# Kernel tuning notes

Measured on AMD Instinct MI355X. Metric: run time of the kernel, lower is better.

The kernel has to match this reference:

```python
import jax, jax.numpy as jnp
import numpy as np

T, N, XD, H, Z, E = 6, 4096, 64, 256, 128, 131072


def setup_inputs() -> dict:
    key = jax.random.key(0)
    ks = jax.random.split(key, 16)
    f32 = jnp.float32
    def rn(k, shp):
        return jax.random.normal(k, shp, f32)
    def gl(k, shp):  # glorot-ish init, scaled by fan_in
        return jax.random.normal(k, shp, f32) * np.float32(1.0 / np.sqrt(shp[-2]))
    return {
        "x": rn(ks[0], (T, N, XD)),
        "edges": jax.random.randint(ks[1], (T, 2, E), 0, N, dtype=jnp.int32),
        "eps": rn(ks[2], (T, N, Z)),
        "drop_u": jax.random.uniform(ks[3], (T, N, Z), f32),
        "phi_x_w": gl(ks[4], (XD, H)), "phi_x_b": jnp.zeros((H,), f32),
        "phi_z_w": gl(ks[5], (Z, H)), "phi_z_b": jnp.zeros((H,), f32),
        "enc_w": gl(ks[6], (2 * H, H)),
        "enc_mu_w": gl(ks[7], (H, Z)),
        "enc_lv_w": gl(ks[8], (H, Z)),
        "prior_w": gl(ks[9], (H, H)), "prior_b": jnp.zeros((H,), f32),
        "prior_mu_w": gl(ks[10], (H, Z)), "prior_mu_b": jnp.zeros((Z,), f32),
        "prior_lv_w": gl(ks[11], (H, Z)), "prior_lv_b": jnp.zeros((Z,), f32),
        "gru_wx": gl(ks[12], (4, 2 * H, H)),  # gates i,f,o,c; x-side GCN weights
        "gru_wh": gl(ks[13], (4, H, H)),      # gates i,f,o,c; h-side GCN weights
    }


def reference(x, edges, eps, drop_u, phi_x_w, phi_x_b, phi_z_w, phi_z_b,
              enc_w, enc_mu_w, enc_lv_w, prior_w, prior_b,
              prior_mu_w, prior_mu_b, prior_lv_w, prior_lv_b,
              gru_wx, gru_wh):
    T_, N_, _ = x.shape
    H_ = phi_x_w.shape[1]
    h = jnp.zeros((N_, H_), x.dtype)
    c = jnp.zeros((N_, H_), x.dtype)
    loop = jnp.arange(N_, dtype=edges.dtype)
    enc_mus, prior_mus = [], []
    dec_t = None
    for t in range(T_):  # fixed small T; edge structure differs per step
        row = jnp.concatenate([edges[t, 0], loop])  # add self loops
        col = jnp.concatenate([edges[t, 1], loop])
        deg = jax.ops.segment_sum(jnp.ones(row.shape, x.dtype), row, num_segments=N_)
        dinv = jnp.where(deg > 0, jax.lax.rsqrt(deg), jnp.zeros((), x.dtype))
        norm = (dinv[row] * dinv[col])[:, None]

        def gcn(xx, W):
            # GCNConv: xW, gather at col, scale by sym-norm, scatter-add at row
            return jax.ops.segment_sum(norm * (xx @ W)[col], row, num_segments=N_)

        phi_x_t = jax.nn.relu(x[t] @ phi_x_w + phi_x_b)
        enc_t = jax.nn.relu(gcn(jnp.concatenate([phi_x_t, h], axis=1), enc_w))
        enc_mu_t = gcn(enc_t, enc_mu_w)
        enc_std_t = jax.nn.softplus(gcn(enc_t, enc_lv_w))
        prior_t = jax.nn.relu(h @ prior_w + prior_b)
        prior_mu_t = prior_t @ prior_mu_w + prior_mu_b
        _prior_std_t = jax.nn.softplus(prior_t @ prior_lv_w + prior_lv_b)  # computed as in original, unused in returns
        z_t = eps[t] * enc_std_t + enc_mu_t  # original: eps.mul(logvar).add_(mu)
        phi_z_t = jax.nn.relu(z_t @ phi_z_w + phi_z_b)
        # InnerProductDecoder with dropout(p=0.5, training=True), identity act
        z_drop = jnp.where(drop_u[t] < 0.5, z_t * 2.0, jnp.zeros((), x.dtype))
        dec_t = z_drop @ z_drop.T  # [N, N]
        # graph-LSTM step (n_layer = 1)
        xin = jnp.concatenate([phi_x_t, phi_z_t], axis=1)  # [N, 2H]
        gi = jax.nn.sigmoid(gcn(xin, gru_wx[0]) + gcn(h, gru_wh[0]))
        gf = jax.nn.sigmoid(gcn(xin, gru_wx[1]) + gcn(h, gru_wh[1]))
        go = jax.nn.sigmoid(gcn(xin, gru_wx[2]) + gcn(h, gru_wh[2]))
        ct = jnp.tanh(gcn(xin, gru_wx[3]) + gcn(h, gru_wh[3]))
        c_new = gf * h + gi * ct    # faithful to original: F_g * h[i] (not c)
        h_new = go * jnp.tanh(c)    # faithful to original: uses old c[i]
        h, c = h_new, c_new
        enc_mus.append(enc_mu_t)
        prior_mus.append(prior_mu_t)
    return jnp.stack(enc_mus), jnp.stack(prior_mus), h[None], dec_t
```

## Files before the change

kernel.cpp:

```cpp
#include <hip/hip_runtime.h>
#include <hip/hip_bf16.h>
#include <math.h>

#define T_  6
#define NN  4096
#define XD_ 64
#define H_  256
#define ZZ  128
#define EE  131072

typedef unsigned short u16;
typedef __attribute__((ext_vector_type(8))) short short8;
typedef __attribute__((ext_vector_type(8))) unsigned short u16x8;
typedef __attribute__((ext_vector_type(4))) float f32x4;

__device__ __forceinline__ float bf2f(u16 u) { return __uint_as_float(((unsigned)u) << 16); }
__device__ __forceinline__ u16 f2bf(float f) {
    unsigned x = __float_as_uint(f);
    return (u16)((x + 0x7FFFu + ((x >> 16) & 1u)) >> 16);
}

__global__ void k_deg(const int* __restrict__ edges, int* __restrict__ degcnt) {
    int t = blockIdx.y;
    int e = blockIdx.x * 256 + threadIdx.x;
    const int* rows = edges + (size_t)t * 2 * EE;
    atomicAdd(&degcnt[t * NN + rows[e]], 1);
}

__global__ void k_scan_dinv(const int* __restrict__ degcnt_all,
                            int* __restrict__ row_start_all,
                            int* __restrict__ cursor_all,
                            float* __restrict__ dinv_all) {
    __shared__ int sbuf[1024];
    int tt = blockIdx.x;
    const int* degcnt = degcnt_all + tt * NN;
    int* row_start = row_start_all + tt * (NN + 1);
    int* cursor = cursor_all + tt * NN;
    float* dinv = dinv_all + tt * NN;
    int t = threadIdx.x;
    int b = t * 4;
    int v0 = degcnt[b + 0], v1 = degcnt[b + 1], v2 = degcnt[b + 2], v3 = degcnt[b + 3];
    dinv[b + 0] = rsqrtf((float)(v0 + 1));
    dinv[b + 1] = rsqrtf((float)(v1 + 1));
    dinv[b + 2] = rsqrtf((float)(v2 + 1));
    dinv[b + 3] = rsqrtf((float)(v3 + 1));
    int s = v0 + v1 + v2 + v3;
    sbuf[t] = s;
    __syncthreads();
    for (int off = 1; off < 1024; off <<= 1) {
        int x = sbuf[t];
        int y = (t >= off) ? sbuf[t - off] : 0;
        __syncthreads();
        sbuf[t] = x + y;
        __syncthreads();
    }
    int excl = sbuf[t] - s;
    int r0 = excl, r1 = excl + v0, r2 = r1 + v1, r3 = r2 + v2;
    row_start[b + 0] = r0; cursor[b + 0] = r0;
    row_start[b + 1] = r1; cursor[b + 1] = r1;
    row_start[b + 2] = r2; cursor[b + 2] = r2;
    row_start[b + 3] = r3; cursor[b + 3] = r3;
    if (t == 1023) row_start[NN] = r3 + v3;
}

__global__ void k_scatter(const int* __restrict__ edges,
                          int* __restrict__ cursor, const float* __restrict__ dinv,
                          int* __restrict__ col_idx, float* __restrict__ val) {
    int t = blockIdx.y;
    int e = blockIdx.x * 256 + threadIdx.x;
    const int* rows = edges + (size_t)t * 2 * EE;
    const int* cols = rows + EE;
    int r = rows[e], cc = cols[e];
    int pos = atomicAdd(&cursor[t * NN + r], 1);
    col_idx[(size_t)t * EE + pos] = cc;
    val[(size_t)t * EE + pos] = dinv[t * NN + r] * dinv[t * NN + cc];
}

__device__ __forceinline__ void sp_row_wave(const u16* __restrict__ Y,
                                            const int* __restrict__ row_start,
                                            const int* __restrict__ col_idx,
                                            const float* __restrict__ val,
                                            const float* __restrict__ dinv,
                                            u16* __restrict__ outp, int ldo, int r) {
    int lane = threadIdx.x & 63;
    int half = lane >> 5;
    int cg = lane & 31;
    int s0 = row_start[r], s1 = row_start[r + 1];
    float a[8] = {0.f, 0.f, 0.f, 0.f, 0.f, 0.f, 0.f, 0.f};
    for (int base = s0; base < s1; base += 64) {
        int n = s1 - base; if (n > 64) n = 64;
        int cl = 0; float vl = 0.f;
        if (base + lane < s1) { cl = col_idx[base + lane]; vl = val[base + lane]; }
        for (int e = 0; e < n; e += 2) {
            int ei = e + half;
            int cc = __shfl(cl, ei);
            float v = (ei < n) ? __shfl(vl, ei) : 0.f;
            u16x8 y = *(const u16x8*)(Y + (size_t)cc * H_ + cg * 8);
#pragma unroll
            for (int j = 0; j < 8; ++j) a[j] += v * bf2f(y[j]);
        }
    }
#pragma unroll
    for (int j = 0; j < 8; ++j) a[j] += __shfl_xor(a[j], 32);
    if (half == 0) {
        float dr = dinv[r], sc = dr * dr;
        u16x8 ys = *(const u16x8*)(Y + (size_t)r * H_ + cg * 8);
        u16x8 o;
#pragma unroll
        for (int j = 0; j < 8; ++j) o[j] = f2bf(a[j] + sc * bf2f(ys[j]));
        *(u16x8*)(outp + (size_t)r * ldo + cg * 8) = o;
    }
}

__global__ void k_spmm(const u16* __restrict__ Y1,
                       const int* __restrict__ row_start_all, const int* __restrict__ col_idx_all,
                       const float* __restrict__ val_all, const float* __restrict__ dinv_all,
                       u16* __restrict__ out1, int ldo,
                       long long sY, long long sO) {
    int t = blockIdx.y;
    int w = threadIdx.x >> 6;
    sp_row_wave(Y1 + (size_t)t * sY, row_start_all + (size_t)t * (NN + 1),
                col_idx_all + (size_t)t * EE, val_all + (size_t)t * EE,
                dinv_all + (size_t)t * NN, out1 + (size_t)t * sO, ldo,
                blockIdx.x * 4 + w);
}

template<int MF>
__device__ __forceinline__ void mm_core(const u16* __restrict__ A, int lda,
                                        const u16* __restrict__ BT, int ldbt, int K,
                                        int row0, int col0,
                                        f32x4 acc[MF][MF], char* smem) {
    constexpr int TILE = MF * 32;
    u16* As = (u16*)smem;
    u16* Bs = As + TILE * 64;
    const int lane = threadIdx.x & 63;
    const int w = threadIdx.x >> 6;
    const int wr = (w >> 1) * (TILE / 2);
    const int wc = (w & 1) * (TILE / 2);

    int gRow[MF], gCol[MF];
#pragma unroll
    for (int i = 0; i < MF; ++i) {
        int G = (w * MF + i) * 64 + lane;
        int r = G >> 3;
        gRow[i] = r;
        gCol[i] = ((G & 7) ^ (r & 7)) << 3;
    }

    for (int k0 = 0; k0 < K; k0 += 64) {
#pragma unroll
        for (int i = 0; i < MF; ++i) {
            const u16* sa = A + (size_t)(row0 + gRow[i]) * lda + k0 + gCol[i];
            __builtin_amdgcn_global_load_lds(
                (const __attribute__((address_space(1))) void*)sa,
                (__attribute__((address_space(3))) void*)(As + (w * MF + i) * 512), 16, 0, 0);
            const u16* sb = BT + (size_t)(col0 + gRow[i]) * ldbt + k0 + gCol[i];
            __builtin_amdgcn_global_load_lds(
                (const __attribute__((address_space(1))) void*)sb,
                (__attribute__((address_space(3))) void*)(Bs + (w * MF + i) * 512), 16, 0, 0);
        }
        __syncthreads();
#pragma unroll
        for (int kk = 0; kk < 2; ++kk) {
            short8 a[MF], b[MF];
#pragma unroll
            for (int mf = 0; mf < MF; ++mf) {
                int r = wr + mf * 16 + (lane & 15);
                int off = (r * 128 + kk * 64 + (lane >> 4) * 16) ^ ((r & 7) << 4);
                a[mf] = *(const short8*)((const char*)As + off);
            }
#pragma unroll
            for (int nf = 0; nf < MF; ++nf) {
                int r = wc + nf * 16 + (lane & 15);
                int off = (r * 128 + kk * 64 + (lane >> 4) * 16) ^ ((r & 7) << 4);
                b[nf] = *(const short8*)((const char*)Bs + off);
            }
#pragma unroll
            for (int mf = 0; mf < MF; ++mf)
#pragma unroll
                for (int nf = 0; nf < MF; ++nf)
                    acc[mf][nf] = __builtin_amdgcn_mfma_f32_16x16x32_bf16(
                        a[mf], b[nf], acc[mf][nf], 0, 0, 0);
        }
        __syncthreads();
    }
}

template<int MF>
__launch_bounds__(256)
__global__ void k_mm(const u16* __restrict__ A, int lda,
                     const u16* __restrict__ BT, int ldbt, int K,
                     float* __restrict__ C0, int ldc0,
                     u16* __restrict__ C1, int ldc1,
                     const float* __restrict__ bias, int act,
                     float* __restrict__ C2,
                     const float* __restrict__ du, u16* __restrict__ zdOut) {
    constexpr int TILE = MF * 32;
    constexpr int STAGE_B = TILE * 64 * 2 * 2;
    constexpr int EPI_B = (MF == 2) ? 64 * 68 * 4 : 0;
    constexpr int SMEM_B = STAGE_B > EPI_B ? STAGE_B : EPI_B;
    __shared__ alignas(16) char smem[SMEM_B];

    const int tid = threadIdx.x;
    const int lane = tid & 63;
    const int w = tid >> 6;
    const int row0 = blockIdx.y * TILE;
    const int col0 = blockIdx.x * TILE;
    const int wr = (w >> 1) * (TILE / 2);
    const int wc = (w & 1) * (TILE / 2);

    f32x4 acc[MF][MF];
#pragma unroll
    for (int i = 0; i < MF; ++i)
#pragma unroll
        for (int j = 0; j < MF; ++j)
            acc[i][j] = f32x4{0.f, 0.f, 0.f, 0.f};

    mm_core<MF>(A, lda, BT, ldbt, K, row0, col0, acc, smem);

    const int ci = lane & 15;
    const int ri = (lane >> 4) * 4;

    if constexpr (MF == 2) {
        if (act == 4) {
            float (*epi)[68] = (float(*)[68])smem;
#pragma unroll
            for (int mf = 0; mf < 2; ++mf)
#pragma unroll
                for (int nf = 0; nf < 2; ++nf)
#pragma unroll
                    for (int i = 0; i < 4; ++i)
                        epi[wr + mf * 16 + ri + i][wc + nf * 16 + ci] = acc[mf][nf][i];
            __syncthreads();
            float* muo = C0; const float* eps = C2; u16* zo = C1;
#pragma unroll
            for (int k = 0; k < 8; ++k) {
                int p = tid + k * 256;
                int row = p >> 5, jl = p & 31;
                float mu = epi[row][jl * 2];
                float sp = epi[row][jl * 2 + 1];
                float sd = (sp > 20.f) ? sp : log1pf(expf(sp));
                int idx = (row0 + row) * ZZ + (col0 >> 1) + jl;
                muo[idx] = mu;
                u16 z16 = f2bf(eps[idx] * sd + mu);
                zo[idx] = z16;
                if (zdOut)
                    zdOut[idx] = (du[idx] < 0.5f) ? f2bf(2.f * bf2f(z16)) : (u16)0;
            }
            return;
        }
    }

#pragma unroll
    for (int mf = 0; mf < MF; ++mf) {
#pragma unroll
        for (int nf = 0; nf < MF; ++nf) {
            int row = row0 + wr + mf * 16 + ri;
            int col = col0 + wc + nf * 16 + ci;
            if (C1) {
                float bv = bias ? bias[col] : 0.f;
#pragma unroll
                for (int i = 0; i < 4; ++i) {
                    float v = acc[mf][nf][i] + bv;
                    if (act == 1) v = fmaxf(v, 0.f);
                    C1[(size_t)(row + i) * ldc1 + col] = f2bf(v);
                }
            } else {
                float bv = bias ? bias[col] : 0.f;
#pragma unroll
                for (int i = 0; i < 4; ++i)
                    C0[(size_t)(row + i) * ldc0 + col] = acc[mf][nf][i] + bv;
            }
        }
    }
}

__launch_bounds__(256)
__global__ void k_dual(const u16* __restrict__ A0, int lda0, const u16* __restrict__ BT0,
                       int ldbt0, int K0, u16* __restrict__ Cb0, int ldcb0,
                       const u16* __restrict__ A1, int lda1, const u16* __restrict__ BT1,
                       int ldbt1, int K1, float* __restrict__ Cf1, int ldcf1,
                       const float* __restrict__ bias1) {
    __shared__ alignas(16) char smem[16384];
    const int z = blockIdx.z;
    if (z && blockIdx.x >= 2) return;
    const u16* A = z ? A1 : A0;   int lda = z ? lda1 : lda0;
    const u16* BT = z ? BT1 : BT0; int ldbt = z ? ldbt1 : ldbt0;
    int K = z ? K1 : K0;

    const int lane = threadIdx.x & 63;
    const int w = threadIdx.x >> 6;
    const int row0 = blockIdx.y * 64;
    const int col0 = blockIdx.x * 64;
    const int wr = (w >> 1) * 32, wc = (w & 1) * 32;

    f32x4 acc[2][2];
#pragma unroll
    for (int i = 0; i < 2; ++i)
#pragma unroll
        for (int j = 0; j < 2; ++j) acc[i][j] = f32x4{0.f, 0.f, 0.f, 0.f};
    mm_core<2>(A, lda, BT, ldbt, K, row0, col0, acc, smem);

    const int ci = lane & 15, ri = (lane >> 4) * 4;
#pragma unroll
    for (int mf = 0; mf < 2; ++mf)
#pragma unroll
        for (int nf = 0; nf < 2; ++nf) {
            int row = row0 + wr + mf * 16 + ri;
            int col = col0 + wc + nf * 16 + ci;
            if (z == 0) {
#pragma unroll
                for (int i = 0; i < 4; ++i)
                    Cb0[(size_t)(row + i) * ldcb0 + col] = f2bf(fmaxf(acc[mf][nf][i], 0.f));
            } else {
                float bv = bias1[col];
#pragma unroll
                for (int i = 0; i < 4; ++i)
                    Cf1[(size_t)(row + i) * ldcf1 + col] = acc[mf][nf][i] + bv;
            }
        }
}

__launch_bounds__(256)
__global__ void k_sp_mm(const u16* __restrict__ Y, const int* __restrict__ row_start,
                        const int* __restrict__ col_idx, const float* __restrict__ val,
                        const float* __restrict__ dinv, u16* __restrict__ spOut, int spLdo,
                        int doSp,
                        const u16* __restrict__ A, int lda, const u16* __restrict__ BT,
                        int ldbt, int K, float* __restrict__ Cf, int ldcf,
                        u16* __restrict__ Cb, int ldcb,
                        const float* __restrict__ bias, int gx) {
    __shared__ alignas(16) char smem[16384];
    int bid = blockIdx.x;
    if (bid < NN / 4) {
        if (!doSp) return;
        int w = threadIdx.x >> 6;
        sp_row_wave(Y, row_start, col_idx, val, dinv, spOut, spLdo, bid * 4 + w);
        return;
    }
    int b2 = bid - NN / 4;
    const int row0 = (b2 / gx) * 64;
    const int col0 = (b2 % gx) * 64;
    const int lane = threadIdx.x & 63;
    const int w = threadIdx.x >> 6;
    const int wr = (w >> 1) * 32, wc = (w & 1) * 32;
    f32x4 acc[2][2];
#pragma unroll
    for (int i = 0; i < 2; ++i)
#pragma unroll
        for (int j = 0; j < 2; ++j) acc[i][j] = f32x4{0.f, 0.f, 0.f, 0.f};
    mm_core<2>(A, lda, BT, ldbt, K, row0, col0, acc, smem);
    const int ci = lane & 15, ri = (lane >> 4) * 4;
#pragma unroll
    for (int mf = 0; mf < 2; ++mf)
#pragma unroll
        for (int nf = 0; nf < 2; ++nf) {
            int row = row0 + wr + mf * 16 + ri;
            int col = col0 + wc + nf * 16 + ci;
            float bv = bias ? bias[col] : 0.f;
            if (Cb) {
#pragma unroll
                for (int i = 0; i < 4; ++i)
                    Cb[(size_t)(row + i) * ldcb + col] = f2bf(fmaxf(acc[mf][nf][i] + bv, 0.f));
            } else {
#pragma unroll
                for (int i = 0; i < 4; ++i)
                    Cf[(size_t)(row + i) * ldcf + col] = acc[mf][nf][i] + bv;
            }
        }
}

__launch_bounds__(256)
__global__ void k_gates(const u16* __restrict__ XIN, const u16* __restrict__ BgT,
                        float* __restrict__ h, float* __restrict__ c,
                        u16* __restrict__ hbf, float* __restrict__ hOut,
                        int skipSH) {
    __shared__ alignas(16) char smem[128 * 68 * 4];
    u16* As = (u16*)smem;
    u16* Bs = As + 128 * 64;
    const int tid = threadIdx.x;
    const int lane = tid & 63;
    const int w = tid >> 6;
    const int row0 = blockIdx.y * 128;
    const int col0 = blockIdx.x * 64;
    const int wrB = (w >> 1) * 64;
    const int wc = (w & 1) * 32;

    f32x4 acc[4][2];
#pragma unroll
    for (int i = 0; i < 4; ++i)
#pragma unroll
        for (int j = 0; j < 2; ++j) acc[i][j] = f32x4{0.f, 0.f, 0.f, 0.f};

    int aRow[4], aCol[4];
#pragma unroll
    for (int i = 0; i < 4; ++i) {
        int G = (w * 4 + i) * 64 + lane;
        int r = G >> 3;
        aRow[i] = r;
        aCol[i] = ((G & 7) ^ (r & 7)) << 3;
    }
    int bRow[2], bCol[2];
#pragma unroll
    for (int i = 0; i < 2; ++i) {
        int G = (w * 2 + i) * 64 + lane;
        int r = G >> 3;
        bRow[i] = r;
        bCol[i] = ((G & 7) ^ (r & 7)) << 3;
    }

    const int nIter = skipSH ? 8 : 12;
    for (int it = 0; it < nIter; ++it) {
        int k0 = it * 64 + ((skipSH && it >= 4) ? 256 : 0);
#pragma unroll
        for (int i = 0; i < 4; ++i) {
            const u16* sa = XIN + (size_t)(row0 + aRow[i]) * 768 + k0 + aCol[i];
            __builtin_amdgcn_global_load_lds(
                (const __attribute__((address_space(1))) void*)sa,
                (__attribute__((address_space(3))) void*)(As + (w * 4 + i) * 512), 16, 0, 0);
        }
#pragma unroll
        for (int i = 0; i < 2; ++i) {
            const u16* sb = BgT + (size_t)(col0 + bRow[i]) * 768 + k0 + bCol[i];
            __builtin_amdgcn_global_load_lds(
                (const __attribute__((address_space(1))) void*)sb,
                (__attribute__((address_space(3))) void*)(Bs + (w * 2 + i) * 512), 16, 0, 0);
        }
        __syncthreads();
#pragma unroll
        for (int kk = 0; kk < 2; ++kk) {
            short8 a[4], b[2];
#pragma unroll
            for (int mf = 0; mf < 4; ++mf) {
                int r = wrB + mf * 16 + (lane & 15);
                int off = (r * 128 + kk * 64 + (lane >> 4) * 16) ^ ((r & 7) << 4);
                a[mf] = *(const short8*)((const char*)As + off);
            }
#pragma unroll
            for (int nf = 0; nf < 2; ++nf) {
                int r = wc + nf * 16 + (lane & 15);
                int off = (r * 128 + kk * 64 + (lane >> 4) * 16) ^ ((r & 7) << 4);
                b[nf] = *(const short8*)((const char*)Bs + off);
            }
#pragma unroll
            for (int mf = 0; mf < 4; ++mf)
#pragma unroll
                for (int nf = 0; nf < 2; ++nf)
                    acc[mf][nf] = __builtin_amdgcn_mfma_f32_16x16x32_bf16(
                        a[mf], b[nf], acc[mf][nf], 0, 0, 0);
        }
        __syncthreads();
    }

    const int ci = lane & 15;
    const int ri = (lane >> 4) * 4;
    float (*epi)[68] = (float(*)[68])smem;
#pragma unroll
    for (int mf = 0; mf < 4; ++mf)
#pragma unroll
        for (int nf = 0; nf < 2; ++nf)
#pragma unroll
            for (int i = 0; i < 4; ++i)
                epi[wrB + mf * 16 + ri + i][wc + nf * 16 + ci] = acc[mf][nf][i];
    __syncthreads();
#pragma unroll
    for (int k = 0; k < 8; ++k) {
        int p = tid + k * 256;
        int row = p >> 4, jl = p & 15;
        float4 g4 = *(const float4*)&epi[row][jl * 4];
        float gi = 1.f / (1.f + expf(-g4.x));
        float gf = 1.f / (1.f + expf(-g4.y));
        float go = 1.f / (1.f + expf(-g4.z));
        float ct = tanhf(g4.w);
        int idx = (row0 + row) * H_ + (col0 >> 2) + jl;
        float ho = h[idx], co = c[idx];
        float cn = gf * ho + gi * ct;
        float hn = go * tanhf(co);
        h[idx] = hn;
        c[idx] = cn;
        hbf[idx] = f2bf(hn);
        if (hOut) hOut[idx] = hn;
    }
}

__global__ void k_cvt(const float* __restrict__ in, u16* __restrict__ outp, int n4) {
    int i = blockIdx.x * 256 + threadIdx.x;
    if (i >= n4) return;
    float4 v = ((const float4*)in)[i];
    ((ushort4*)outp)[i] = make_ushort4(f2bf(v.x), f2bf(v.y), f2bf(v.z), f2bf(v.w));
}

__global__ void k_prep(const float* __restrict__ phi_x_w, const float* __restrict__ phi_z_w,
                       const float* __restrict__ enc_w, const float* __restrict__ prior_w,
                       const float* __restrict__ prior_mu_w,
                       const float* __restrict__ enc_mu_w, const float* __restrict__ enc_lv_w,
                       const float* __restrict__ gru_wx, const float* __restrict__ gru_wh,
                       u16* __restrict__ phi_x_wT, u16* __restrict__ phi_z_wT,
                       u16* __restrict__ enc_wT, u16* __restrict__ prior_wT,
                       u16* __restrict__ prior_mu_wT, u16* __restrict__ mulvT,
                       u16* __restrict__ BgT) {
    int idx = blockIdx.x * 256 + threadIdx.x;
    if (idx < 16384) {
        int j = idx >> 6, k = idx & 63;
        phi_x_wT[idx] = f2bf(phi_x_w[k * 256 + j]);
        return;
    }
    idx -= 16384;
    if (idx < 32768) {
        int j = idx >> 7, k = idx & 127;
        phi_z_wT[idx] = f2bf(phi_z_w[k * 256 + j]);
        return;
    }
    idx -= 32768;
    if (idx < 131072) {
        int j = idx >> 9, k = idx & 511;
        enc_wT[idx] = f2bf(enc_w[k * 256 + j]);
        return;
    }
    idx -= 131072;
    if (idx < 65536) {
        int j = idx >> 8, k = idx & 255;
        prior_wT[idx] = f2bf(prior_w[k * 256 + j]);
        return;
    }
    idx -= 65536;
    if (idx < 32768) {
        int j = idx >> 8, k = idx & 255;
        prior_mu_wT[idx] = f2bf(prior_mu_w[k * 128 + j]);
        return;
    }
    idx -= 32768;
    if (idx < 65536) {
        int cp = idx >> 8, k = idx & 255;
        int j = cp >> 1, s = cp & 1;
        float v = s ? enc_lv_w[k * 128 + j] : enc_mu_w[k * 128 + j];
        mulvT[idx] = f2bf(v);
        return;
    }
    idx -= 65536;
    if (idx < 786432) {
        int cp = idx / 768, k = idx % 768;
        int g = cp & 3, j = cp >> 2;
        float v;
        if (k < 256)      v = gru_wx[((size_t)g * 512 + k) * 256 + j];
        else if (k < 512) v = gru_wh[((size_t)g * 256 + (k - 256)) * 256 + j];
        else              v = gru_wx[((size_t)g * 512 + (k - 256)) * 256 + j];
        BgT[idx] = f2bf(v);
    }
}

extern "C" void kernel_launch(void* const* d_in, const int* in_sizes, int n_in,
                              void* d_out_v, int out_size, void* d_ws, size_t ws_size,
                              hipStream_t stream) {
    (void)in_sizes; (void)n_in; (void)out_size;
    const float* x          = (const float*)d_in[0];
    const int*   edges      = (const int*)d_in[1];
    const float* eps        = (const float*)d_in[2];
    const float* drop_u     = (const float*)d_in[3];
    const float* phi_x_w    = (const float*)d_in[4];
    const float* phi_x_b    = (const float*)d_in[5];
    const float* phi_z_w    = (const float*)d_in[6];
    const float* phi_z_b    = (const float*)d_in[7];
    const float* enc_w      = (const float*)d_in[8];
    const float* enc_mu_w   = (const float*)d_in[9];
    const float* enc_lv_w   = (const float*)d_in[10];
    const float* prior_w    = (const float*)d_in[11];
    const float* prior_b    = (const float*)d_in[12];
    const float* prior_mu_w = (const float*)d_in[13];
    const float* prior_mu_b = (const float*)d_in[14];
    const float* gru_wx     = (const float*)d_in[17];
    const float* gru_wh     = (const float*)d_in[18];
    float* out = (float*)d_out_v;

    char* base = (char*)d_ws;
    size_t cur = 0;
    auto carve = [&](size_t bytes) -> void* {
        void* p = base + cur;
        cur += (bytes + 255) & ~(size_t)255;
        return p;
    };
    float* h         = (float*)carve((size_t)NN * H_ * 4);
    float* c         = (float*)carve((size_t)NN * H_ * 4);
    u16* h_bf        = (u16*)carve((size_t)NN * H_ * 2);
    size_t hcz_bytes = cur;
    float* dinv      = (float*)carve((size_t)T_ * NN * 4);
    int*   degcnt    = (int*)carve((size_t)T_ * NN * 4);
    int*   row_start = (int*)carve((size_t)T_ * (NN + 1) * 4);
    int*   cursor    = (int*)carve((size_t)T_ * NN * 4);
    int*   col_idx   = (int*)carve((size_t)T_ * EE * 4);
    float* val       = (float*)carve((size_t)T_ * EE * 4);
    u16* x_bf        = (u16*)carve((size_t)T_ * NN * XD_ * 2);
    u16* phi6        = (u16*)carve((size_t)T_ * NN * H_ * 2);
    u16* phi         = (u16*)carve((size_t)NN * H_ * 2);
    u16* enc_t       = (u16*)carve((size_t)NN * H_ * 2);
    u16* SEb         = (u16*)carve((size_t)NN * H_ * 2);
    u16* prior_t     = (u16*)carve((size_t)NN * H_ * 2);
    u16* XIN6        = (u16*)carve((size_t)T_ * NN * 768 * 2);
    u16* zbuf        = (u16*)carve((size_t)NN * ZZ * 2);
    u16* zd          = (u16*)carve((size_t)NN * ZZ * 2);
    u16* phi_x_wT    = (u16*)carve((size_t)XD_ * H_ * 2);
    u16* phi_z_wT    = (u16*)carve((size_t)ZZ * H_ * 2);
    u16* enc_wT      = (u16*)carve((size_t)512 * H_ * 2);
    u16* prior_wT    = (u16*)carve((size_t)H_ * H_ * 2);
    u16* prior_mu_wT = (u16*)carve((size_t)ZZ * H_ * 2);
    u16* mulvT       = (u16*)carve((size_t)H_ * H_ * 2);
    u16* BgT         = (u16*)carve((size_t)1024 * 768 * 2);
    if (cur > ws_size) return;

    const size_t NZ = (size_t)NN * ZZ;
    const size_t HOFF = (size_t)2 * T_ * NZ;
    const size_t DECOFF = HOFF + (size_t)NN * H_;

    k_cvt<<<(T_ * NN * XD_ / 4 + 255) / 256, 256, 0, stream>>>(x, x_bf, T_ * NN * XD_ / 4);
    k_prep<<<(1130496 + 255) / 256, 256, 0, stream>>>(
        phi_x_w, phi_z_w, enc_w, prior_w, prior_mu_w, enc_mu_w, enc_lv_w,
        gru_wx, gru_wh,
        phi_x_wT, phi_z_wT, enc_wT, prior_wT, prior_mu_wT, mulvT, BgT);

    hipMemsetAsync(degcnt, 0, (size_t)T_ * NN * 4, stream);
    k_deg<<<dim3(EE / 256, T_), 256, 0, stream>>>(edges, degcnt);
    k_scan_dinv<<<T_, 1024, 0, stream>>>(degcnt, row_start, cursor, dinv);
    k_scatter<<<dim3(EE / 256, T_), 256, 0, stream>>>(edges, cursor, dinv, col_idx, val);

    k_mm<2><<<dim3(4, (T_ * NN) / 64), 256, 0, stream>>>(x_bf, XD_, phi_x_wT, XD_, XD_,
        nullptr, 0, phi6, H_, phi_x_b, 1, nullptr, nullptr, nullptr);
    k_spmm<<<dim3(NN / 4, T_), 256, 0, stream>>>(phi6, row_start, col_idx, val, dinv,
        XIN6, 768, (long long)NN * H_, (long long)NN * 768);

    hipMemsetAsync(h, 0, hcz_bytes, stream);

    for (int t = 0; t < T_; ++t) {
        const int* rs_t = row_start + (size_t)t * (NN + 1);
        const int* ci_t = col_idx + (size_t)t * EE;
        const float* vv_t = val + (size_t)t * EE;
        const float* dv_t = dinv + (size_t)t * NN;
        u16* xin_t = XIN6 + (size_t)t * NN * 768;
        int last = (t == T_ - 1);

        k_sp_mm<<<NN / 4 + 256, 256, 0, stream>>>(h_bf, rs_t, ci_t, vv_t, dv_t,
            xin_t + 256, 768, t > 0,
            h_bf, H_, prior_wT, H_, H_, nullptr, 0, prior_t, H_, prior_b, 4);
        k_dual<<<dim3(4, 64, 2), 256, 0, stream>>>(
            xin_t, 768, enc_wT, 512, (t == 0) ? 256 : 512, enc_t, H_,
            prior_t, H_, prior_mu_wT, H_, H_,
            out + (size_t)(T_ + t) * NZ, ZZ, prior_mu_b);
        k_spmm<<<dim3(NN / 4, 1), 256, 0, stream>>>(enc_t, rs_t, ci_t, vv_t, dv_t,
                                                    SEb, H_, 0, 0);
        k_mm<2><<<dim3(4, 64), 256, 0, stream>>>(SEb, H_, mulvT, H_, H_,
            out + (size_t)t * NZ, 0, zbuf, 0, nullptr, 4, (float*)(eps + (size_t)t * NZ),
            last ? drop_u + (size_t)t * NZ : nullptr, last ? zd : nullptr);
        k_mm<2><<<dim3(4, 64), 256, 0, stream>>>(zbuf, ZZ, phi_z_wT, ZZ, ZZ,
            nullptr, 0, phi, H_, phi_z_b, 1, nullptr, nullptr, nullptr);
        k_spmm<<<dim3(NN / 4, 1), 256, 0, stream>>>(phi, rs_t, ci_t, vv_t, dv_t,
                                                    xin_t + 512, 768, 0, 0);
        k_gates<<<dim3(16, 32), 256, 0, stream>>>(xin_t, BgT, h, c, h_bf,
            last ? out + HOFF : nullptr, t == 0);
    }

    k_mm<4><<<dim3(32, 32), 256, 0, stream>>>(zd, ZZ, zd, ZZ, ZZ,
        out + DECOFF, NN, nullptr, 0, nullptr, 0, nullptr, nullptr, nullptr);
}
```

Baseline: 611.1 us.

## Fuse per-timestep kernel chain into one cooperative persistent kernel with grid syncs

Replaces the sequence of roughly seven kernel launches per timestep with a single cooperative kernel that loops over timesteps and stages, separating stages with grid-wide syncs. It also folds the x conversion and the degree memset into the weight-prep kernel. The aim is to remove launch overhead and inter-kernel gaps across the serial recurrence. The cost is that each stage is limited to a fixed grid of 256 or 512 blocks, grid.sync has its own overhead, and a non-cooperative fallback path is kept.

```diff
diff --git a/kernel.cpp b/kernel.cpp
--- a/kernel.cpp
+++ b/kernel.cpp
@@ -1,6 +1,8 @@
 #include <hip/hip_runtime.h>
-#include <hip/hip_bf16.h>
+#include <hip/hip_cooperative_groups.h>
 #include <math.h>
+
+namespace cg = cooperative_groups;
 
 #define T_  6
 #define NN  4096
@@ -84,7 +86,7 @@
                                             u16* __restrict__ outp, int ldo, int r) {
     int lane = threadIdx.x & 63;
     int half = lane >> 5;
-    int cg = lane & 31;
+    int cg2 = lane & 31;
     int s0 = row_start[r], s1 = row_start[r + 1];
     float a[8] = {0.f, 0.f, 0.f, 0.f, 0.f, 0.f, 0.f, 0.f};
     for (int base = s0; base < s1; base += 64) {
@@ -95,7 +97,7 @@
             int ei = e + half;
             int cc = __shfl(cl, ei);
             float v = (ei < n) ? __shfl(vl, ei) : 0.f;
-            u16x8 y = *(const u16x8*)(Y + (size_t)cc * H_ + cg * 8);
+            u16x8 y = *(const u16x8*)(Y + (size_t)cc * H_ + cg2 * 8);
 #pragma unroll
             for (int j = 0; j < 8; ++j) a[j] += v * bf2f(y[j]);
         }
@@ -104,11 +106,11 @@
     for (int j = 0; j < 8; ++j) a[j] += __shfl_xor(a[j], 32);
     if (half == 0) {
         float dr = dinv[r], sc = dr * dr;
-        u16x8 ys = *(const u16x8*)(Y + (size_t)r * H_ + cg * 8);
+        u16x8 ys = *(const u16x8*)(Y + (size_t)r * H_ + cg2 * 8);
         u16x8 o;
 #pragma unroll
         for (int j = 0; j < 8; ++j) o[j] = f2bf(a[j] + sc * bf2f(ys[j]));
-        *(u16x8*)(outp + (size_t)r * ldo + cg * 8) = o;
+        *(u16x8*)(outp + (size_t)r * ldo + cg2 * 8) = o;
     }
 }
 
@@ -186,170 +188,18 @@
     }
 }
 
-template<int MF>
-__launch_bounds__(256)
-__global__ void k_mm(const u16* __restrict__ A, int lda,
-                     const u16* __restrict__ BT, int ldbt, int K,
-                     float* __restrict__ C0, int ldc0,
-                     u16* __restrict__ C1, int ldc1,
-                     const float* __restrict__ bias, int act,
-                     float* __restrict__ C2,
-                     const float* __restrict__ du, u16* __restrict__ zdOut) {
-    constexpr int TILE = MF * 32;
-    constexpr int STAGE_B = TILE * 64 * 2 * 2;
-    constexpr int EPI_B = (MF == 2) ? 64 * 68 * 4 : 0;
-    constexpr int SMEM_B = STAGE_B > EPI_B ? STAGE_B : EPI_B;
-    __shared__ alignas(16) char smem[SMEM_B];
-
-    const int tid = threadIdx.x;
-    const int lane = tid & 63;
-    const int w = tid >> 6;
-    const int row0 = blockIdx.y * TILE;
-    const int col0 = blockIdx.x * TILE;
-    const int wr = (w >> 1) * (TILE / 2);
-    const int wc = (w & 1) * (TILE / 2);
-
-    f32x4 acc[MF][MF];
-#pragma unroll
-    for (int i = 0; i < MF; ++i)
-#pragma unroll
-        for (int j = 0; j < MF; ++j)
-            acc[i][j] = f32x4{0.f, 0.f, 0.f, 0.f};
-
-    mm_core<MF>(A, lda, BT, ldbt, K, row0, col0, acc, smem);
-
-    const int ci = lane & 15;
-    const int ri = (lane >> 4) * 4;
-
-    if constexpr (MF == 2) {
-        if (act == 4) {
-            float (*epi)[68] = (float(*)[68])smem;
-#pragma unroll
-            for (int mf = 0; mf < 2; ++mf)
-#pragma unroll
-                for (int nf = 0; nf < 2; ++nf)
-#pragma unroll
-                    for (int i = 0; i < 4; ++i)
-                        epi[wr + mf * 16 + ri + i][wc + nf * 16 + ci] = acc[mf][nf][i];
-            __syncthreads();
-            float* muo = C0; const float* eps = C2; u16* zo = C1;
-#pragma unroll
-            for (int k = 0; k < 8; ++k) {
-                int p = tid + k * 256;
-                int row = p >> 5, jl = p & 31;
-                float mu = epi[row][jl * 2];
-                float sp = epi[row][jl * 2 + 1];
-                float sd = (sp > 20.f) ? sp : log1pf(expf(sp));
-                int idx = (row0 + row) * ZZ + (col0 >> 1) + jl;
-                muo[idx] = mu;
-                u16 z16 = f2bf(eps[idx] * sd + mu);
-                zo[idx] = z16;
-                if (zdOut)
-                    zdOut[idx] = (du[idx] < 0.5f) ? f2bf(2.f * bf2f(z16)) : (u16)0;
-            }
-            return;
-        }
-    }
-
-#pragma unroll
-    for (int mf = 0; mf < MF; ++mf) {
-#pragma unroll
-        for (int nf = 0; nf < MF; ++nf) {
-            int row = row0 + wr + mf * 16 + ri;
-            int col = col0 + wc + nf * 16 + ci;
-            if (C1) {
-                float bv = bias ? bias[col] : 0.f;
-#pragma unroll
-                for (int i = 0; i < 4; ++i) {
-                    float v = acc[mf][nf][i] + bv;
-                    if (act == 1) v = fmaxf(v, 0.f);
-                    C1[(size_t)(row + i) * ldc1 + col] = f2bf(v);
-                }
-            } else {
-                float bv = bias ? bias[col] : 0.f;
-#pragma unroll
-                for (int i = 0; i < 4; ++i)
-                    C0[(size_t)(row + i) * ldc0 + col] = acc[mf][nf][i] + bv;
-            }
-        }
-    }
-}
-
-__launch_bounds__(256)
-__global__ void k_dual(const u16* __restrict__ A0, int lda0, const u16* __restrict__ BT0,
-                       int ldbt0, int K0, u16* __restrict__ Cb0, int ldcb0,
-                       const u16* __restrict__ A1, int lda1, const u16* __restrict__ BT1,
-                       int ldbt1, int K1, float* __restrict__ Cf1, int ldcf1,
-                       const float* __restrict__ bias1) {
-    __shared__ alignas(16) char smem[16384];
-    const int z = blockIdx.z;
-    if (z && blockIdx.x >= 2) return;
-    const u16* A = z ? A1 : A0;   int lda = z ? lda1 : lda0;
-    const u16* BT = z ? BT1 : BT0; int ldbt = z ? ldbt1 : ldbt0;
-    int K = z ? K1 : K0;
-
-    const int lane = threadIdx.x & 63;
-    const int w = threadIdx.x >> 6;
-    const int row0 = blockIdx.y * 64;
-    const int col0 = blockIdx.x * 64;
+__device__ __forceinline__ void zacc2(f32x4 acc[2][2]) {
+#pragma unroll
+    for (int i = 0; i < 2; ++i)
+#pragma unroll
+        for (int j = 0; j < 2; ++j) acc[i][j] = f32x4{0.f, 0.f, 0.f, 0.f};
+}
+
+__device__ __forceinline__ void epi_bf16relu(f32x4 acc[2][2], u16* __restrict__ C,
+                                             int ldc, int row0, int col0,
+                                             const float* __restrict__ bias) {
+    const int lane = threadIdx.x & 63, w = threadIdx.x >> 6;
     const int wr = (w >> 1) * 32, wc = (w & 1) * 32;
-
-    f32x4 acc[2][2];
-#pragma unroll
-    for (int i = 0; i < 2; ++i)
-#pragma unroll
-        for (int j = 0; j < 2; ++j) acc[i][j] = f32x4{0.f, 0.f, 0.f, 0.f};
-    mm_core<2>(A, lda, BT, ldbt, K, row0, col0, acc, smem);
-
-    const int ci = lane & 15, ri = (lane >> 4) * 4;
-#pragma unroll
-    for (int mf = 0; mf < 2; ++mf)
-#pragma unroll
-        for (int nf = 0; nf < 2; ++nf) {
-            int row = row0 + wr + mf * 16 + ri;
-            int col = col0 + wc + nf * 16 + ci;
-            if (z == 0) {
-#pragma unroll
-                for (int i = 0; i < 4; ++i)
-                    Cb0[(size_t)(row + i) * ldcb0 + col] = f2bf(fmaxf(acc[mf][nf][i], 0.f));
-            } else {
-                float bv = bias1[col];
-#pragma unroll
-                for (int i = 0; i < 4; ++i)
-                    Cf1[(size_t)(row + i) * ldcf1 + col] = acc[mf][nf][i] + bv;
-            }
-        }
-}
-
-__launch_bounds__(256)
-__global__ void k_sp_mm(const u16* __restrict__ Y, const int* __restrict__ row_start,
-                        const int* __restrict__ col_idx, const float* __restrict__ val,
-                        const float* __restrict__ dinv, u16* __restrict__ spOut, int spLdo,
-                        int doSp,
-                        const u16* __restrict__ A, int lda, const u16* __restrict__ BT,
-                        int ldbt, int K, float* __restrict__ Cf, int ldcf,
-                        u16* __restrict__ Cb, int ldcb,
-                        const float* __restrict__ bias, int gx) {
-    __shared__ alignas(16) char smem[16384];
-    int bid = blockIdx.x;
-    if (bid < NN / 4) {
-        if (!doSp) return;
-        int w = threadIdx.x >> 6;
-        sp_row_wave(Y, row_start, col_idx, val, dinv, spOut, spLdo, bid * 4 + w);
-        return;
-    }
-    int b2 = bid - NN / 4;
-    const int row0 = (b2 / gx) * 64;
-    const int col0 = (b2 % gx) * 64;
-    const int lane = threadIdx.x & 63;
-    const int w = threadIdx.x >> 6;
-    const int wr = (w >> 1) * 32, wc = (w & 1) * 32;
-    f32x4 acc[2][2];
-#pragma unroll
-    for (int i = 0; i < 2; ++i)
-#pragma unroll
-        for (int j = 0; j < 2; ++j) acc[i][j] = f32x4{0.f, 0.f, 0.f, 0.f};
-    mm_core<2>(A, lda, BT, ldbt, K, row0, col0, acc, smem);
     const int ci = lane & 15, ri = (lane >> 4) * 4;
 #pragma unroll
     for (int mf = 0; mf < 2; ++mf)
@@ -358,31 +208,43 @@
             int row = row0 + wr + mf * 16 + ri;
             int col = col0 + wc + nf * 16 + ci;
             float bv = bias ? bias[col] : 0.f;
-            if (Cb) {
-#pragma unroll
-                for (int i = 0; i < 4; ++i)
-                    Cb[(size_t)(row + i) * ldcb + col] = f2bf(fmaxf(acc[mf][nf][i] + bv, 0.f));
-            } else {
-#pragma unroll
-                for (int i = 0; i < 4; ++i)
-                    Cf[(size_t)(row + i) * ldcf + col] = acc[mf][nf][i] + bv;
-            }
-        }
-}
-
-__launch_bounds__(256)
-__global__ void k_gates(const u16* __restrict__ XIN, const u16* __restrict__ BgT,
-                        float* __restrict__ h, float* __restrict__ c,
-                        u16* __restrict__ hbf, float* __restrict__ hOut,
-                        int skipSH) {
-    __shared__ alignas(16) char smem[128 * 68 * 4];
+#pragma unroll
+            for (int i = 0; i < 4; ++i)
+                C[(size_t)(row + i) * ldc + col] = f2bf(fmaxf(acc[mf][nf][i] + bv, 0.f));
+        }
+}
+
+__device__ __forceinline__ void epi_f32b(f32x4 acc[2][2], float* __restrict__ C,
+                                         int ldc, int row0, int col0,
+                                         const float* __restrict__ bias) {
+    const int lane = threadIdx.x & 63, w = threadIdx.x >> 6;
+    const int wr = (w >> 1) * 32, wc = (w & 1) * 32;
+    const int ci = lane & 15, ri = (lane >> 4) * 4;
+#pragma unroll
+    for (int mf = 0; mf < 2; ++mf)
+#pragma unroll
+        for (int nf = 0; nf < 2; ++nf) {
+            int row = row0 + wr + mf * 16 + ri;
+            int col = col0 + wc + nf * 16 + ci;
+            float bv = bias[col];
+#pragma unroll
+            for (int i = 0; i < 4; ++i)
+                C[(size_t)(row + i) * ldc + col] = acc[mf][nf][i] + bv;
+        }
+}
+
+__device__ __forceinline__ void gates_tile(const u16* __restrict__ XIN,
+                                           const u16* __restrict__ BgT,
+                                           float* __restrict__ h, float* __restrict__ c,
+                                           u16* __restrict__ hbf, float* __restrict__ hOut,
+                                           int skipSH, int tt, char* smem) {
     u16* As = (u16*)smem;
     u16* Bs = As + 128 * 64;
     const int tid = threadIdx.x;
     const int lane = tid & 63;
     const int w = tid >> 6;
-    const int row0 = blockIdx.y * 128;
-    const int col0 = blockIdx.x * 64;
+    const int row0 = (tt >> 4) * 128;
+    const int col0 = (tt & 15) * 64;
     const int wrB = (w >> 1) * 64;
     const int wc = (w & 1) * 32;
 
@@ -481,13 +343,149 @@
         hbf[idx] = f2bf(hn);
         if (hOut) hOut[idx] = hn;
     }
-}
-
-__global__ void k_cvt(const float* __restrict__ in, u16* __restrict__ outp, int n4) {
-    int i = blockIdx.x * 256 + threadIdx.x;
-    if (i >= n4) return;
-    float4 v = ((const float4*)in)[i];
-    ((ushort4*)outp)[i] = make_ushort4(f2bf(v.x), f2bf(v.y), f2bf(v.z), f2bf(v.w));
+    __syncthreads();
+}
+
+template<int MF>
+__launch_bounds__(256)
+__global__ void k_mm(const u16* __restrict__ A, int lda,
+                     const u16* __restrict__ BT, int ldbt, int K,
+                     float* __restrict__ C0, int ldc0,
+                     u16* __restrict__ C1, int ldc1,
+                     const float* __restrict__ bias, int act,
+                     float* __restrict__ C2,
+                     const float* __restrict__ du, u16* __restrict__ zdOut) {
+    constexpr int TILE = MF * 32;
+    constexpr int STAGE_B = TILE * 64 * 2 * 2;
+    constexpr int EPI_B = (MF == 2) ? 64 * 68 * 4 : 0;
+    constexpr int SMEM_B = STAGE_B > EPI_B ? STAGE_B : EPI_B;
+    __shared__ alignas(16) char smem[SMEM_B];
+
+    const int tid = threadIdx.x;
+    const int lane = tid & 63;
+    const int w = tid >> 6;
+    const int row0 = blockIdx.y * TILE;
+    const int col0 = blockIdx.x * TILE;
+    const int wr = (w >> 1) * (TILE / 2);
+    const int wc = (w & 1) * (TILE / 2);
+
+    f32x4 acc[MF][MF];
+#pragma unroll
+    for (int i = 0; i < MF; ++i)
+#pragma unroll
+        for (int j = 0; j < MF; ++j)
+            acc[i][j] = f32x4{0.f, 0.f, 0.f, 0.f};
+
+    mm_core<MF>(A, lda, BT, ldbt, K, row0, col0, acc, smem);
+
+    const int ci = lane & 15;
+    const int ri = (lane >> 4) * 4;
+
+    if constexpr (MF == 2) {
+        if (act == 4) {
+            float (*epi)[68] = (float(*)[68])smem;
+#pragma unroll
+            for (int mf = 0; mf < 2; ++mf)
+#pragma unroll
+                for (int nf = 0; nf < 2; ++nf)
+#pragma unroll
+                    for (int i = 0; i < 4; ++i)
+                        epi[wr + mf * 16 + ri + i][wc + nf * 16 + ci] = acc[mf][nf][i];
+            __syncthreads();
+            float* muo = C0; const float* eps = C2; u16* zo = C1;
+#pragma unroll
+            for (int k = 0; k < 8; ++k) {
+                int p = tid + k * 256;
+                int row = p >> 5, jl = p & 31;
+                float mu = epi[row][jl * 2];
+                float sp = epi[row][jl * 2 + 1];
+                float sd = (sp > 20.f) ? sp : log1pf(expf(sp));
+                int idx = (row0 + row) * ZZ + (col0 >> 1) + jl;
+                muo[idx] = mu;
+                u16 z16 = f2bf(eps[idx] * sd + mu);
+                zo[idx] = z16;
+                if (zdOut)
+                    zdOut[idx] = (du[idx] < 0.5f) ? f2bf(2.f * bf2f(z16)) : (u16)0;
+            }
+            return;
+        }
+    }
+
+#pragma unroll
+    for (int mf = 0; mf < MF; ++mf) {
+#pragma unroll
+        for (int nf = 0; nf < MF; ++nf) {
+            int row = row0 + wr + mf * 16 + ri;
+            int col = col0 + wc + nf * 16 + ci;
+            if (C1) {
+                float bv = bias ? bias[col] : 0.f;
+#pragma unroll
+                for (int i = 0; i < 4; ++i) {
+                    float v = acc[mf][nf][i] + bv;
+                    if (act == 1) v = fmaxf(v, 0.f);
+                    C1[(size_t)(row + i) * ldc1 + col] = f2bf(v);
+                }
+            } else {
+                float bv = bias ? bias[col] : 0.f;
+#pragma unroll
+                for (int i = 0; i < 4; ++i)
+                    C0[(size_t)(row + i) * ldc0 + col] = acc[mf][nf][i] + bv;
+            }
+        }
+    }
+}
+
+__launch_bounds__(256)
+__global__ void k_dual(const u16* __restrict__ A0, int lda0, const u16* __restrict__ BT0,
+                       int ldbt0, int K0, u16* __restrict__ Cb0, int ldcb0,
+                       const u16* __restrict__ A1, int lda1, const u16* __restrict__ BT1,
+                       int ldbt1, int K1, float* __restrict__ Cf1, int ldcf1,
+                       const float* __restrict__ bias1) {
+    __shared__ alignas(16) char smem[16384];
+    const int z = blockIdx.z;
+    if (z && blockIdx.x >= 2) return;
+    const u16* A = z ? A1 : A0;   int lda = z ? lda1 : lda0;
+    const u16* BT = z ? BT1 : BT0; int ldbt = z ? ldbt1 : ldbt0;
+    int K = z ? K1 : K0;
+    const int row0 = blockIdx.y * 64;
+    const int col0 = blockIdx.x * 64;
+    f32x4 acc[2][2]; zacc2(acc);
+    mm_core<2>(A, lda, BT, ldbt, K, row0, col0, acc, smem);
+    if (z == 0) epi_bf16relu(acc, Cb0, ldcb0, row0, col0, nullptr);
+    else        epi_f32b(acc, Cf1, ldcf1, row0, col0, bias1);
+}
+
+__launch_bounds__(256)
+__global__ void k_sp_mm(const u16* __restrict__ Y, const int* __restrict__ row_start,
+                        const int* __restrict__ col_idx, const float* __restrict__ val,
+                        const float* __restrict__ dinv, u16* __restrict__ spOut, int spLdo,
+                        int doSp,
+                        const u16* __restrict__ A, int lda, const u16* __restrict__ BT,
+                        int ldbt, int K, u16* __restrict__ Cb, int ldcb,
+                        const float* __restrict__ bias, int gx) {
+    __shared__ alignas(16) char smem[16384];
+    int bid = blockIdx.x;
+    if (bid < NN / 4) {
+        if (!doSp) return;
+        int w = threadIdx.x >> 6;
+        sp_row_wave(Y, row_start, col_idx, val, dinv, spOut, spLdo, bid * 4 + w);
+        return;
+    }
+    int b2 = bid - NN / 4;
+    const int row0 = (b2 / gx) * 64;
+    const int col0 = (b2 % gx) * 64;
+    f32x4 acc[2][2]; zacc2(acc);
+    mm_core<2>(A, lda, BT, ldbt, K, row0, col0, acc, smem);
+    epi_bf16relu(acc, Cb, ldcb, row0, col0, bias);
+}
+
+__launch_bounds__(256)
+__global__ void k_gates(const u16* __restrict__ XIN, const u16* __restrict__ BgT,
+                        float* __restrict__ h, float* __restrict__ c,
+                        u16* __restrict__ hbf, float* __restrict__ hOut,
+                        int skipSH) {
+    __shared__ alignas(16) char smem[34816];
+    gates_tile(XIN, BgT, h, c, hbf, hOut, skipSH, blockIdx.y * 16 + blockIdx.x, smem);
 }
 
 __global__ void k_prep(const float* __restrict__ phi_x_w, const float* __restrict__ phi_z_w,
@@ -498,7 +496,9 @@
                        u16* __restrict__ phi_x_wT, u16* __restrict__ phi_z_wT,
                        u16* __restrict__ enc_wT, u16* __restrict__ prior_wT,
                        u16* __restrict__ prior_mu_wT, u16* __restrict__ mulvT,
-                       u16* __restrict__ BgT) {
+                       u16* __restrict__ BgT,
+                       const float* __restrict__ x, u16* __restrict__ x_bf,
+                       int* __restrict__ degcnt) {
     int idx = blockIdx.x * 256 + threadIdx.x;
     if (idx < 16384) {
         int j = idx >> 6, k = idx & 63;
@@ -546,6 +546,166 @@
         else if (k < 512) v = gru_wh[((size_t)g * 256 + (k - 256)) * 256 + j];
         else              v = gru_wx[((size_t)g * 512 + (k - 256)) * 256 + j];
         BgT[idx] = f2bf(v);
+        return;
+    }
+    idx -= 786432;
+    if (idx < 393216) {
+        float4 v = ((const float4*)x)[idx];
+        ((ushort4*)x_bf)[idx] = make_ushort4(f2bf(v.x), f2bf(v.y), f2bf(v.z), f2bf(v.w));
+        return;
+    }
+    idx -= 393216;
+    if (idx < 6144)
+        ((int4*)degcnt)[idx] = make_int4(0, 0, 0, 0);
+}
+
+struct MegaArgs {
+    const u16 *x_bf, *phi_x_wT;
+    const float *phi_x_b;
+    u16 *phi6, *XIN6;
+    const int *row_start, *col_idx;
+    const float *val, *dinv;
+    float *hcz;
+    float *h, *c; u16 *h_bf;
+    const u16 *enc_wT; u16 *enc_t;
+    const u16 *prior_wT; const float *prior_b; u16 *prior_t;
+    const u16 *prior_mu_wT; const float *prior_mu_b;
+    const u16 *mulvT;
+    const float *eps, *drop_u;
+    u16 *zbuf, *zd;
+    const u16 *phi_z_wT; const float *phi_z_b; u16 *phiz;
+    u16 *SEb;
+    const u16 *BgT;
+    float *out;
+};
+
+__launch_bounds__(256, 2)
+__global__ void k_mega(MegaArgs a) {
+    cg::grid_group grid = cg::this_grid();
+    __shared__ alignas(16) char smem[34816];
+    const int bid = blockIdx.x;
+    const int G = gridDim.x;
+    const int tid = threadIdx.x;
+    const int w = tid >> 6;
+    const size_t NZ = (size_t)NN * ZZ;
+    const size_t HOFF = 2 * (size_t)T_ * NZ;
+
+    {
+        float4* z4 = (float4*)a.hcz;
+        for (int i = bid * 256 + tid; i < 655360; i += G * 256)
+            z4[i] = make_float4(0.f, 0.f, 0.f, 0.f);
+        for (int tt = bid; tt < 1536; tt += G) {
+            int row0 = (tt >> 2) * 64, col0 = (tt & 3) * 64;
+            f32x4 acc[2][2]; zacc2(acc);
+            mm_core<2>(a.x_bf, XD_, a.phi_x_wT, XD_, XD_, row0, col0, acc, smem);
+            epi_bf16relu(acc, a.phi6, H_, row0, col0, a.phi_x_b);
+        }
+    }
+    grid.sync();
+
+    for (int r = bid * 4 + w; r < T_ * NN; r += G * 4) {
+        int t = r >> 12, rr = r & (NN - 1);
+        sp_row_wave(a.phi6 + (size_t)t * NN * H_, a.row_start + t * (NN + 1),
+                    a.col_idx + (size_t)t * EE, a.val + (size_t)t * EE,
+                    a.dinv + t * NN, a.XIN6 + (size_t)t * NN * 768, 768, rr);
+    }
+    grid.sync();
+
+    for (int t = 0; t < T_; ++t) {
+        const int* rs = a.row_start + t * (NN + 1);
+        const int* cidx = a.col_idx + (size_t)t * EE;
+        const float* vv = a.val + (size_t)t * EE;
+        const float* dv = a.dinv + t * NN;
+        u16* xin = a.XIN6 + (size_t)t * NN * 768;
+        const int last = (t == T_ - 1);
+        const int half = G >> 1;
+
+        if (bid < half) {
+            for (int tt = bid; tt < 256; tt += half) {
+                int row0 = (tt >> 2) * 64, col0 = (tt & 3) * 64;
+                f32x4 acc[2][2]; zacc2(acc);
+                mm_core<2>(a.h_bf, H_, a.prior_wT, H_, H_, row0, col0, acc, smem);
+                epi_bf16relu(acc, a.prior_t, H_, row0, col0, a.prior_b);
+            }
+        } else if (t > 0) {
+            for (int r = (bid - half) * 4 + w; r < NN; r += half * 4)
+                sp_row_wave(a.h_bf, rs, cidx, vv, dv, xin + 256, 768, r);
+        }
+        grid.sync();
+
+        for (int tt = bid; tt < 384; tt += G) {
+            if (tt < 256) {
+                int row0 = (tt >> 2) * 64, col0 = (tt & 3) * 64;
+                f32x4 acc[2][2]; zacc2(acc);
+                mm_core<2>(xin, 768, a.enc_wT, 512, t ? 512 : 256, row0, col0, acc, smem);
+                epi_bf16relu(acc, a.enc_t, H_, row0, col0, nullptr);
+            } else {
+                int b2 = tt - 256;
+                int row0 = (b2 >> 1) * 64, col0 = (b2 & 1) * 64;
+                f32x4 acc[2][2]; zacc2(acc);
+                mm_core<2>(a.prior_t, H_, a.prior_mu_wT, H_, H_, row0, col0, acc, smem);
+                epi_f32b(acc, a.out + (size_t)(T_ + t) * NZ, ZZ, row0, col0, a.prior_mu_b);
+            }
+            __syncthreads();
+        }
+        grid.sync();
+
+        for (int r = bid * 4 + w; r < NN; r += G * 4)
+            sp_row_wave(a.enc_t, rs, cidx, vv, dv, a.SEb, H_, r);
+        grid.sync();
+
+        for (int tt = bid; tt < 256; tt += G) {
+            int row0 = (tt >> 2) * 64, col0 = (tt & 3) * 64;
+            f32x4 acc[2][2]; zacc2(acc);
+            mm_core<2>(a.SEb, H_, a.mulvT, H_, H_, row0, col0, acc, smem);
+            const int lane = tid & 63;
+            const int wr = (w >> 1) * 32, wc = (w & 1) * 32;
+            const int ci = lane & 15, ri = (lane >> 4) * 4;
+            float (*epi)[68] = (float(*)[68])smem;
+#pragma unroll
+            for (int mf = 0; mf < 2; ++mf)
+#pragma unroll
+                for (int nf = 0; nf < 2; ++nf)
+#pragma unroll
+                    for (int i = 0; i < 4; ++i)
+                        epi[wr + mf * 16 + ri + i][wc + nf * 16 + ci] = acc[mf][nf][i];
+            __syncthreads();
+            const float* eps_t = a.eps + (size_t)t * NZ;
+            const float* du = a.drop_u + (size_t)t * NZ;
+            float* muo = a.out + (size_t)t * NZ;
+#pragma unroll
+            for (int k2 = 0; k2 < 8; ++k2) {
+                int p = tid + k2 * 256;
+                int row = p >> 5, jl = p & 31;
+                float mu = epi[row][jl * 2];
+                float sp = epi[row][jl * 2 + 1];
+                float sd = (sp > 20.f) ? sp : log1pf(expf(sp));
+                int idx = (row0 + row) * ZZ + (col0 >> 1) + jl;
+                muo[idx] = mu;
+                u16 z16 = f2bf(eps_t[idx] * sd + mu);
+                a.zbuf[idx] = z16;
+                if (last) a.zd[idx] = (du[idx] < 0.5f) ? f2bf(2.f * bf2f(z16)) : (u16)0;
+            }
+            __syncthreads();
+        }
+        grid.sync();
+
+        for (int tt = bid; tt < 256; tt += G) {
+            int row0 = (tt >> 2) * 64, col0 = (tt & 3) * 64;
+            f32x4 acc[2][2]; zacc2(acc);
+            mm_core<2>(a.zbuf, ZZ, a.phi_z_wT, ZZ, ZZ, row0, col0, acc, smem);
+            epi_bf16relu(acc, a.phiz, H_, row0, col0, a.phi_z_b);
+        }
+        grid.sync();
+
+        for (int r = bid * 4 + w; r < NN; r += G * 4)
+            sp_row_wave(a.phiz, rs, cidx, vv, dv, xin + 512, 768, r);
+        grid.sync();
+
+        for (int tt = bid; tt < 512; tt += G)
+            gates_tile(xin, a.BgT, a.h, a.c, a.h_bf,
+                       last ? a.out + HOFF : nullptr, t == 0, tt, smem);
+        grid.sync();
     }
 }
 
@@ -591,7 +751,7 @@
     float* val       = (float*)carve((size_t)T_ * EE * 4);
     u16* x_bf        = (u16*)carve((size_t)T_ * NN * XD_ * 2);
     u16* phi6        = (u16*)carve((size_t)T_ * NN * H_ * 2);
-    u16* phi         = (u16*)carve((size_t)NN * H_ * 2);
+    u16* phiz        = (u16*)carve((size_t)NN * H_ * 2);
     u16* enc_t       = (u16*)carve((size_t)NN * H_ * 2);
     u16* SEb         = (u16*)carve((size_t)NN * H_ * 2);
     u16* prior_t     = (u16*)carve((size_t)NN * H_ * 2);
@@ -611,50 +771,77 @@
     const size_t HOFF = (size_t)2 * T_ * NZ;
     const size_t DECOFF = HOFF + (size_t)NN * H_;
 
-    k_cvt<<<(T_ * NN * XD_ / 4 + 255) / 256, 256, 0, stream>>>(x, x_bf, T_ * NN * XD_ / 4);
-    k_prep<<<(1130496 + 255) / 256, 256, 0, stream>>>(
+    k_prep<<<(1529856 + 255) / 256, 256, 0, stream>>>(
         phi_x_w, phi_z_w, enc_w, prior_w, prior_mu_w, enc_mu_w, enc_lv_w,
         gru_wx, gru_wh,
-        phi_x_wT, phi_z_wT, enc_wT, prior_wT, prior_mu_wT, mulvT, BgT);
-
-    hipMemsetAsync(degcnt, 0, (size_t)T_ * NN * 4, stream);
+        phi_x_wT, phi_z_wT, enc_wT, prior_wT, prior_mu_wT, mulvT, BgT,
+        x, x_bf, degcnt);
     k_deg<<<dim3(EE / 256, T_), 256, 0, stream>>>(edges, degcnt);
     k_scan_dinv<<<T_, 1024, 0, stream>>>(degcnt, row_start, cursor, dinv);
     k_scatter<<<dim3(EE / 256, T_), 256, 0, stream>>>(edges, cursor, dinv, col_idx, val);
 
-    k_mm<2><<<dim3(4, (T_ * NN) / 64), 256, 0, stream>>>(x_bf, XD_, phi_x_wT, XD_, XD_,
-        nullptr, 0, phi6, H_, phi_x_b, 1, nullptr, nullptr, nullptr);
-    k_spmm<<<dim3(NN / 4, T_), 256, 0, stream>>>(phi6, row_start, col_idx, val, dinv,
-        XIN6, 768, (long long)NN * H_, (long long)NN * 768);
-
-    hipMemsetAsync(h, 0, hcz_bytes, stream);
-
-    for (int t = 0; t < T_; ++t) {
-        const int* rs_t = row_start + (size_t)t * (NN + 1);
-        const int* ci_t = col_idx + (size_t)t * EE;
-        const float* vv_t = val + (size_t)t * EE;
-        const float* dv_t = dinv + (size_t)t * NN;
-        u16* xin_t = XIN6 + (size_t)t * NN * 768;
-        int last = (t == T_ - 1);
-
-        k_sp_mm<<<NN / 4 + 256, 256, 0, stream>>>(h_bf, rs_t, ci_t, vv_t, dv_t,
-            xin_t + 256, 768, t > 0,
-            h_bf, H_, prior_wT, H_, H_, nullptr, 0, prior_t, H_, prior_b, 4);
-        k_dual<<<dim3(4, 64, 2), 256, 0, stream>>>(
-            xin_t, 768, enc_wT, 512, (t == 0) ? 256 : 512, enc_t, H_,
-            prior_t, H_, prior_mu_wT, H_, H_,
-            out + (size_t)(T_ + t) * NZ, ZZ, prior_mu_b);
-        k_spmm<<<dim3(NN / 4, 1), 256, 0, stream>>>(enc_t, rs_t, ci_t, vv_t, dv_t,
-                                                    SEb, H_, 0, 0);
-        k_mm<2><<<dim3(4, 64), 256, 0, stream>>>(SEb, H_, mulvT, H_, H_,
-            out + (size_t)t * NZ, 0, zbuf, 0, nullptr, 4, (float*)(eps + (size_t)t * NZ),
-            last ? drop_u + (size_t)t * NZ : nullptr, last ? zd : nullptr);
-        k_mm<2><<<dim3(4, 64), 256, 0, stream>>>(zbuf, ZZ, phi_z_wT, ZZ, ZZ,
-            nullptr, 0, phi, H_, phi_z_b, 1, nullptr, nullptr, nullptr);
-        k_spmm<<<dim3(NN / 4, 1), 256, 0, stream>>>(phi, rs_t, ci_t, vv_t, dv_t,
-                                                    xin_t + 512, 768, 0, 0);
-        k_gates<<<dim3(16, 32), 256, 0, stream>>>(xin_t, BgT, h, c, h_bf,
-            last ? out + HOFF : nullptr, t == 0);
+    MegaArgs ma;
+    ma.x_bf = x_bf; ma.phi_x_wT = phi_x_wT; ma.phi_x_b = phi_x_b;
+    ma.phi6 = phi6; ma.XIN6 = XIN6;
+    ma.row_start = row_start; ma.col_idx = col_idx; ma.val = val; ma.dinv = dinv;
+    ma.hcz = h;
+    ma.h = h; ma.c = c; ma.h_bf = h_bf;
+    ma.enc_wT = enc_wT; ma.enc_t = enc_t;
+    ma.prior_wT = prior_wT; ma.prior_b = prior_b; ma.prior_t = prior_t;
+    ma.prior_mu_wT = prior_mu_wT; ma.prior_mu_b = prior_mu_b;
+    ma.mulvT = mulvT;
+    ma.eps = eps; ma.drop_u = drop_u;
+    ma.zbuf = zbuf; ma.zd = zd;
+    ma.phi_z_wT = phi_z_wT; ma.phi_z_b = phi_z_b; ma.phiz = phiz;
+    ma.SEb = SEb;
+    ma.BgT = BgT;
+    ma.out = out;
+    void* params[] = {&ma};
+
+    int maxB = 0;
+    hipError_t qerr = hipOccupancyMaxActiveBlocksPerMultiprocessor(&maxB, k_mega, 256, 0);
+    hipError_t lerr = hipErrorUnknown;
+    if (qerr == hipSuccess && maxB >= 1) {
+        int gridM = (maxB >= 2) ? 512 : 256;
+        lerr = hipLaunchCooperativeKernel(k_mega, dim3(gridM), dim3(256), params, 0, stream);
+        if (lerr != hipSuccess && gridM == 512)
+            lerr = hipLaunchCooperativeKernel(k_mega, dim3(256), dim3(256), params, 0, stream);
+    }
+
+    if (lerr != hipSuccess) {
+        k_mm<2><<<dim3(4, (T_ * NN) / 64), 256, 0, stream>>>(x_bf, XD_, phi_x_wT, XD_, XD_,
+            nullptr, 0, phi6, H_, phi_x_b, 1, nullptr, nullptr, nullptr);
+        k_spmm<<<dim3(NN / 4, T_), 256, 0, stream>>>(phi6, row_start, col_idx, val, dinv,
+            XIN6, 768, (long long)NN * H_, (long long)NN * 768);
+        hipMemsetAsync(h, 0, hcz_bytes, stream);
+
+        for (int t = 0; t < T_; ++t) {
+            const int* rs_t = row_start + (size_t)t * (NN + 1);
+            const int* ci_t = col_idx + (size_t)t * EE;
+            const float* vv_t = val + (size_t)t * EE;
+            const float* dv_t = dinv + (size_t)t * NN;
+            u16* xin_t = XIN6 + (size_t)t * NN * 768;
+            int last = (t == T_ - 1);
+
+            k_sp_mm<<<NN / 4 + 256, 256, 0, stream>>>(h_bf, rs_t, ci_t, vv_t, dv_t,
+                xin_t + 256, 768, t > 0,
+                h_bf, H_, prior_wT, H_, H_, prior_t, H_, prior_b, 4);
+            k_dual<<<dim3(4, 64, 2), 256, 0, stream>>>(
+                xin_t, 768, enc_wT, 512, (t == 0) ? 256 : 512, enc_t, H_,
+                prior_t, H_, prior_mu_wT, H_, H_,
+                out + (size_t)(T_ + t) * NZ, ZZ, prior_mu_b);
+            k_spmm<<<dim3(NN / 4, 1), 256, 0, stream>>>(enc_t, rs_t, ci_t, vv_t, dv_t,
+                                                        SEb, H_, 0, 0);
+            k_mm<2><<<dim3(4, 64), 256, 0, stream>>>(SEb, H_, mulvT, H_, H_,
+                out + (size_t)t * NZ, 0, zbuf, 0, nullptr, 4, (float*)(eps + (size_t)t * NZ),
+                last ? drop_u + (size_t)t * NZ : nullptr, last ? zd : nullptr);
+            k_mm<2><<<dim3(4, 64), 256, 0, stream>>>(zbuf, ZZ, phi_z_wT, ZZ, ZZ,
+                nullptr, 0, phiz, H_, phi_z_b, 1, nullptr, nullptr, nullptr);
+            k_spmm<<<dim3(NN / 4, 1), 256, 0, stream>>>(phiz, rs_t, ci_t, vv_t, dv_t,
+                                                        xin_t + 512, 768, 0, 0);
+            k_gates<<<dim3(16, 32), 256, 0, stream>>>(xin_t, BgT, h, c, h_bf,
+                last ? out + HOFF : nullptr, t == 0);
+        }
     }
 
     k_mm<4><<<dim3(32, 32), 256, 0, stream>>>(zd, ZZ, zd, ZZ, ZZ,
```

Measured after the change: 2.373 ms. 288% more time.
